# Kernel tuning notes

Hardware: AMD Instinct MI355X
Metric: run time of the kernel (lower is better)

Reference implementation:

```python
import jax, jax.numpy as jnp
import numpy as np

B, L, F, H, DIM = 32, 1024, 1024, 1024, 1024


def setup_inputs() -> dict:
    key = jax.random.key(0)
    ks = jax.random.split(key, 8)
    features = jax.random.normal(ks[0], (B, L, F), dtype=jnp.float32)
    hidden = jax.random.normal(ks[1], (B, H), dtype=jnp.float32)
    # Dense layer params (glorot-ish scale)
    W1 = jax.random.normal(ks[2], (F, DIM), dtype=jnp.float32) / np.sqrt(F)
    b1 = jnp.zeros((DIM,), dtype=jnp.float32)
    W2 = jax.random.normal(ks[3], (H, DIM), dtype=jnp.float32) / np.sqrt(H)
    b2 = jnp.zeros((DIM,), dtype=jnp.float32)
    Wp = jax.random.normal(ks[4], (DIM, 1), dtype=jnp.float32) / np.sqrt(DIM)
    bp = jnp.zeros((1,), dtype=jnp.float32)
    return {"features": features, "hidden": hidden, "W1": W1, "b1": b1,
            "W2": W2, "b2": b2, "Wp": Wp, "bp": bp}


def reference(features, hidden, W1, b1, W2, b2, Wp, bp):
    # features: [B, L, F], hidden: [B, H]
    h1 = jnp.einsum('blf,fd->bld', features, W1) + b1          # [B, L, D]
    h2 = (hidden @ W2 + b2)[:, None, :]                         # [B, 1, D]
    att = jnp.tanh(h1 + h2)                                     # [B, L, D]
    score = jnp.einsum('bld,do->blo', att, Wp) + bp             # [B, L, 1]
    attention_weights = jax.nn.softmax(score, axis=1)           # [B, L, 1]
    context_vector = jnp.sum(attention_weights * features, axis=1)  # [B, F]
    return context_vector
```

## Files before the change

### kernel.cpp

```cpp
#include <hip/hip_runtime.h>
#include <hip/hip_bf16.h>


typedef __attribute__((ext_vector_type(8))) __bf16 bf16x8;
typedef __attribute__((ext_vector_type(4))) float f32x4;

#define BM 128
#define BN 128
#define BK 32

static __device__ __forceinline__ ushort f2bf(float x) {
  unsigned u = __float_as_uint(x);
  return (ushort)((u + 0x7fffu + ((u >> 16) & 1u)) >> 16);
}

typedef __attribute__((address_space(1))) void gbl_t;
typedef __attribute__((address_space(3))) void lds_t;
static __device__ __forceinline__ void gl_lds16(const void* g, void* l) {
  __builtin_amdgcn_global_load_lds((gbl_t*)g, (lds_t*)l, 16, 0, 0);
}

static __device__ __forceinline__ bf16x8 cvt8(float4 lo, float4 hi) {
  __hip_bfloat162 c0 = __float22bfloat162_rn({lo.x, lo.y});
  __hip_bfloat162 c1 = __float22bfloat162_rn({lo.z, lo.w});
  __hip_bfloat162 c2 = __float22bfloat162_rn({hi.x, hi.y});
  __hip_bfloat162 c3 = __float22bfloat162_rn({hi.z, hi.w});
  union { int4 i; bf16x8 v; } u;
  u.i.x = *(int*)&c0; u.i.y = *(int*)&c1; u.i.z = *(int*)&c2; u.i.w = *(int*)&c3;
  return u.v;
}

__global__ __launch_bounds__(256) void transpose_w1_kernel(
    const float* __restrict__ W1, ushort* __restrict__ W1T) {
  __shared__ float t[64][65];
  const int tr = blockIdx.y, tc = blockIdx.x, tid = threadIdx.x;
  const int r = tid >> 4;
  const int c4 = (tid & 15) * 4;
#pragma unroll
  for (int p = 0; p < 4; ++p) {
    const int rr = p * 16 + r;
    float4 v = *(const float4*)(W1 + (size_t)(tr * 64 + rr) * 1024 + tc * 64 + c4);
    t[rr][c4] = v.x; t[rr][c4 + 1] = v.y; t[rr][c4 + 2] = v.z; t[rr][c4 + 3] = v.w;
  }
  __syncthreads();
  const int cc = tid >> 3;
  const int r8 = (tid & 7) * 8;
#pragma unroll
  for (int p = 0; p < 2; ++p) {
    const int c = p * 32 + cc;
    ushort tmp[8];
#pragma unroll
    for (int j = 0; j < 8; ++j) tmp[j] = f2bf(t[r8 + j][c]);
    *(int4*)(W1T + (size_t)(tc * 64 + c) * 1024 + tr * 64 + r8) = *(int4*)tmp;
  }
}

__global__ void zero_kernel(float* __restrict__ p) {
  p[(size_t)blockIdx.x * 256 + threadIdx.x] = 0.f;
}

__global__ __launch_bounds__(256) void h2_kernel(
    const float* __restrict__ hidden, const float* __restrict__ W2,
    const float* __restrict__ b2, float* __restrict__ h2p) {
  const int d = blockIdx.x * 256 + threadIdx.x;
  const int b = blockIdx.y;
  const int z = blockIdx.z;
  const int k0 = z * 128;
  __shared__ float h[128];
  if (threadIdx.x < 128) h[threadIdx.x] = hidden[b * 1024 + k0 + threadIdx.x];
  __syncthreads();
  float acc = (z == 0) ? b2[d] : 0.f;
#pragma unroll 8
  for (int k = 0; k < 128; ++k)
    acc += h[k] * W2[(size_t)(k0 + k) * 1024 + d];
  h2p[z * 32768 + b * 1024 + d] = acc;
}

__global__ __launch_bounds__(256) void gemm_score_kernel(
    const float* __restrict__ feat,
    const ushort* __restrict__ w1t,
    const float* __restrict__ b1,
    const float* __restrict__ h2p,
    const float* __restrict__ wp,
    float* __restrict__ score_p) {
  __shared__ float ldsA[BM * BK];
  __shared__ ushort ldsB[BN * BK];
  __shared__ float sred[2][64];
  const int tid = threadIdx.x;
  const int row0 = blockIdx.x * BM;
  const int col0 = blockIdx.y * BN;
  const int b = row0 >> 10;

  const int wave = tid >> 6, lane = tid & 63;
  const int wm = wave & 1, wn = wave >> 1;
  const int lrow = lane & 15;
  const int quad = lane >> 4;

  int a_go[4], a_ls[4];
#pragma unroll
  for (int it = 0; it < 4; ++it) {
    const int slot = wave * 256 + it * 64 + lane;
    const int r = slot >> 3, kc = slot & 7;
    a_go[it] = (row0 + r) * 1024 + (kc ^ (r & 7)) * 4;
    a_ls[it] = (wave * 256 + it * 64) * 16;
  }
  int b_go[2], b_ls[2];
#pragma unroll
  for (int it = 0; it < 2; ++it) {
    const int slot = wave * 128 + it * 64 + lane;
    const int r = slot >> 2, kc = slot & 3;
    b_go[it] = (col0 + r) * 1024 + (kc ^ ((r >> 1) & 3)) * 8;
    b_ls[it] = (wave * 128 + it * 64) * 16;
  }

  f32x4 acc[4][4] = {};

  for (int k0 = 0; k0 < 1024; k0 += BK) {
#pragma unroll
    for (int it = 0; it < 4; ++it)
      gl_lds16(feat + a_go[it] + k0, (char*)ldsA + a_ls[it]);
#pragma unroll
    for (int it = 0; it < 2; ++it)
      gl_lds16(w1t + b_go[it] + k0, (char*)ldsB + b_ls[it]);
    __syncthreads();

    bf16x8 af[4], bfr[4];
#pragma unroll
    for (int i = 0; i < 4; ++i) {
      const int r = wm * 64 + i * 16 + lrow;
      const int s0 = (quad * 2) ^ (r & 7);
      const int s1 = (quad * 2 + 1) ^ (r & 7);
      float4 lo = *(const float4*)&ldsA[r * 32 + s0 * 4];
      float4 hi = *(const float4*)&ldsA[r * 32 + s1 * 4];
      af[i] = cvt8(lo, hi);
    }
#pragma unroll
    for (int j = 0; j < 4; ++j) {
      const int r = wn * 64 + j * 16 + lrow;
      const int s = quad ^ ((r >> 1) & 3);
      bfr[j] = *(const bf16x8*)&ldsB[r * 32 + s * 8];
    }
#pragma unroll
    for (int i = 0; i < 4; ++i)
#pragma unroll
      for (int j = 0; j < 4; ++j)
        acc[i][j] = __builtin_amdgcn_mfma_f32_16x16x32_bf16(
            af[i], bfr[j], acc[i][j], 0, 0, 0);
    __syncthreads();
  }

  float hbv[4], wpv[4];
#pragma unroll
  for (int j = 0; j < 4; ++j) {
    const int d = col0 + wn * 64 + j * 16 + lrow;
    float hv = b1[d];
#pragma unroll
    for (int p = 0; p < 8; ++p) hv += h2p[p * 32768 + b * 1024 + d];
    hbv[j] = hv;
    wpv[j] = wp[d];
  }
  float rsum[4][4];
#pragma unroll
  for (int i = 0; i < 4; ++i) {
#pragma unroll
    for (int r = 0; r < 4; ++r) {
      float s = 0.f;
#pragma unroll
      for (int j = 0; j < 4; ++j)
        s += tanhf(acc[i][j][r] + hbv[j]) * wpv[j];
      s += __shfl_xor(s, 8);
      s += __shfl_xor(s, 4);
      s += __shfl_xor(s, 2);
      s += __shfl_xor(s, 1);
      rsum[i][r] = s;
    }
  }
  if (wn == 1 && lrow == 0) {
#pragma unroll
    for (int i = 0; i < 4; ++i)
#pragma unroll
      for (int r = 0; r < 4; ++r)
        sred[wm][i * 16 + quad * 4 + r] = rsum[i][r];
  }
  __syncthreads();
  if (wn == 0 && lrow == 0) {
#pragma unroll
    for (int i = 0; i < 4; ++i)
#pragma unroll
      for (int r = 0; r < 4; ++r) {
        const int ro = wm * 64 + i * 16 + quad * 4 + r;
        score_p[(size_t)blockIdx.y * 32768 + row0 + ro] =
            rsum[i][r] + sred[wm][ro & 63];
      }
  }
}

__global__ __launch_bounds__(256) void softmax_kernel(
    const float* __restrict__ score_p, float* __restrict__ w) {
  const int b = blockIdx.x, tid = threadIdx.x;
  const int lane = tid & 63, wv = tid >> 6;
  __shared__ float sm[4], ss[4];
  float v[4];
  float mx = -1e30f;
#pragma unroll
  for (int i = 0; i < 4; ++i) {
    const int idx = b * 1024 + i * 256 + tid;
    float s = 0.f;
#pragma unroll
    for (int p = 0; p < 8; ++p) s += score_p[p * 32768 + idx];
    v[i] = s;
    mx = fmaxf(mx, s);
  }
#pragma unroll
  for (int off = 32; off; off >>= 1) mx = fmaxf(mx, __shfl_xor(mx, off));
  if (lane == 0) sm[wv] = mx;
  __syncthreads();
  mx = fmaxf(fmaxf(sm[0], sm[1]), fmaxf(sm[2], sm[3]));
  float sum = 0.f;
#pragma unroll
  for (int i = 0; i < 4; ++i) {
    v[i] = __expf(v[i] - mx);
    sum += v[i];
  }
#pragma unroll
  for (int off = 32; off; off >>= 1) sum += __shfl_xor(sum, off);
  if (lane == 0) ss[wv] = sum;
  __syncthreads();
  const float inv = 1.f / (ss[0] + ss[1] + ss[2] + ss[3]);
#pragma unroll
  for (int i = 0; i < 4; ++i) w[b * 1024 + i * 256 + tid] = v[i] * inv;
}

__global__ __launch_bounds__(256) void context_kernel(
    const float* __restrict__ w, const float* __restrict__ feat,
    float* __restrict__ out) {
  const int b = blockIdx.y;
  const int l0 = blockIdx.x * 32;
  const int f0 = threadIdx.x * 4;
  __shared__ float wl[32];
  if (threadIdx.x < 32) wl[threadIdx.x] = w[b * 1024 + l0 + threadIdx.x];
  __syncthreads();
  const float* fb = feat + (size_t)b * 1048576 + (size_t)l0 * 1024 + f0;
  float a0 = 0.f, a1 = 0.f, a2 = 0.f, a3 = 0.f;
#pragma unroll 8
  for (int l = 0; l < 32; ++l) {
    float4 v = *(const float4*)(fb + (size_t)l * 1024);
    const float wv = wl[l];
    a0 += wv * v.x;
    a1 += wv * v.y;
    a2 += wv * v.z;
    a3 += wv * v.w;
  }
  float* dst = out + b * 1024 + f0;
  atomicAdd(dst + 0, a0);
  atomicAdd(dst + 1, a1);
  atomicAdd(dst + 2, a2);
  atomicAdd(dst + 3, a3);
}

extern "C" void kernel_launch(void* const* d_in, const int* in_sizes, int n_in,
                              void* d_out, int out_size, void* d_ws, size_t ws_size,
                              hipStream_t stream) {
  const float* feat   = (const float*)d_in[0];
  const float* hidden = (const float*)d_in[1];
  const float* W1     = (const float*)d_in[2];
  const float* b1     = (const float*)d_in[3];
  const float* W2     = (const float*)d_in[4];
  const float* b2     = (const float*)d_in[5];
  const float* Wp     = (const float*)d_in[6];
  float* out = (float*)d_out;

  char* ws = (char*)d_ws;
  ushort* w1t    = (ushort*)ws;
  float* score_p = (float*)(ws + 2097152);
  float* h2p     = (float*)(ws + 3145728);
  float* wts     = (float*)(ws + 4194304);

  transpose_w1_kernel<<<dim3(16, 16), 256, 0, stream>>>(W1, w1t);
  h2_kernel<<<dim3(4, 32, 8), 256, 0, stream>>>(hidden, W2, b2, h2p);
  gemm_score_kernel<<<dim3(256, 8), 256, 0, stream>>>(feat, w1t, b1, h2p, Wp,
                                                      score_p);
  softmax_kernel<<<32, 256, 0, stream>>>(score_p, wts);
  zero_kernel<<<128, 256, 0, stream>>>(out);
  context_kernel<<<dim3(32, 32), 256, 0, stream>>>(wts, feat, out);
}
```

Measured before the change: 392.2 us.

## Pre-convert features to bf16 in chunks before GEMM, with register-convert fallback

Adds a pass that converts the fp32 features to bf16 in a workspace buffer, processed in two halves, so the score GEMM can stream bf16 A tiles straight into LDS with half the bytes and no per-tile conversion. When the workspace is too small, a fallback GEMM instead loads fp32 through registers, converts, and writes padded LDS rows. The extra conversion pass adds a full read of features plus a bf16 write, which costs memory traffic. The context kernel still re-reads the fp32 features.

```diff
diff --git a/kernel.cpp b/kernel.cpp
--- a/kernel.cpp
+++ b/kernel.cpp
@@ -8,6 +8,7 @@
 #define BM 128
 #define BN 128
 #define BK 32
+#define LDK 40
 
 static __device__ __forceinline__ ushort f2bf(float x) {
   unsigned u = __float_as_uint(x);
@@ -28,6 +29,17 @@
   union { int4 i; bf16x8 v; } u;
   u.i.x = *(int*)&c0; u.i.y = *(int*)&c1; u.i.z = *(int*)&c2; u.i.w = *(int*)&c3;
   return u.v;
+}
+
+__global__ __launch_bounds__(256) void cvt_feat_kernel(
+    const float* __restrict__ feat, ushort* __restrict__ featb) {
+  const size_t i8 = ((size_t)blockIdx.x * 256 + threadIdx.x) * 8;
+  float4 a = *(const float4*)(feat + i8);
+  float4 b = *(const float4*)(feat + i8 + 4);
+  ushort t[8];
+  t[0] = f2bf(a.x); t[1] = f2bf(a.y); t[2] = f2bf(a.z); t[3] = f2bf(a.w);
+  t[4] = f2bf(b.x); t[5] = f2bf(b.y); t[6] = f2bf(b.z); t[7] = f2bf(b.w);
+  *(int4*)(featb + i8) = *(int4*)t;
 }
 
 __global__ __launch_bounds__(256) void transpose_w1_kernel(
@@ -76,69 +88,96 @@
   h2p[z * 32768 + b * 1024 + d] = acc;
 }
 
-__global__ __launch_bounds__(256) void gemm_score_kernel(
-    const float* __restrict__ feat,
+#define GEMM_EPILOGUE(ROWG)                                                    \
+  float hbv[4], wpv[4];                                                        \
+  _Pragma("unroll") for (int j = 0; j < 4; ++j) {                              \
+    const int d = col0 + wn * 64 + j * 16 + lrow;                              \
+    float hv = b1[d];                                                          \
+    _Pragma("unroll") for (int p = 0; p < 8; ++p)                              \
+        hv += h2p[p * 32768 + b * 1024 + d];                                   \
+    hbv[j] = hv;                                                               \
+    wpv[j] = wp[d];                                                            \
+  }                                                                            \
+  float rsum[4][4];                                                            \
+  _Pragma("unroll") for (int i = 0; i < 4; ++i) {                              \
+    _Pragma("unroll") for (int r = 0; r < 4; ++r) {                            \
+      float s = 0.f;                                                           \
+      _Pragma("unroll") for (int j = 0; j < 4; ++j)                            \
+          s += tanhf(acc[i][j][r] + hbv[j]) * wpv[j];                          \
+      s += __shfl_xor(s, 8);                                                   \
+      s += __shfl_xor(s, 4);                                                   \
+      s += __shfl_xor(s, 2);                                                   \
+      s += __shfl_xor(s, 1);                                                   \
+      rsum[i][r] = s;                                                          \
+    }                                                                          \
+  }                                                                            \
+  if (wn == 1 && lrow == 0) {                                                  \
+    _Pragma("unroll") for (int i = 0; i < 4; ++i)                              \
+        _Pragma("unroll") for (int r = 0; r < 4; ++r)                          \
+            sred[wm][i * 16 + quad * 4 + r] = rsum[i][r];                      \
+  }                                                                            \
+  __syncthreads();                                                             \
+  if (wn == 0 && lrow == 0) {                                                  \
+    _Pragma("unroll") for (int i = 0; i < 4; ++i)                              \
+        _Pragma("unroll") for (int r = 0; r < 4; ++r) {                        \
+          const int ro = wm * 64 + i * 16 + quad * 4 + r;                      \
+          score_p[(size_t)blockIdx.y * 32768 + (ROWG) + ro] =                  \
+              rsum[i][r] + sred[wm][ro & 63];                                  \
+        }                                                                      \
+  }
+
+__global__ __launch_bounds__(256) void gemm_score_bf16_kernel(
+    const ushort* __restrict__ featb,
     const ushort* __restrict__ w1t,
-    const float* __restrict__ b1,
-    const float* __restrict__ h2p,
-    const float* __restrict__ wp,
-    float* __restrict__ score_p) {
-  __shared__ float ldsA[BM * BK];
+    const float* __restrict__ b1, const float* __restrict__ h2p,
+    const float* __restrict__ wp, float* __restrict__ score_p,
+    int row_base) {
+  __shared__ ushort ldsA[BM * BK];
   __shared__ ushort ldsB[BN * BK];
   __shared__ float sred[2][64];
   const int tid = threadIdx.x;
   const int row0 = blockIdx.x * BM;
   const int col0 = blockIdx.y * BN;
-  const int b = row0 >> 10;
+  const int b = (row_base + row0) >> 10;
 
   const int wave = tid >> 6, lane = tid & 63;
   const int wm = wave & 1, wn = wave >> 1;
-  const int lrow = lane & 15;
-  const int quad = lane >> 4;
-
-  int a_go[4], a_ls[4];
-#pragma unroll
-  for (int it = 0; it < 4; ++it) {
-    const int slot = wave * 256 + it * 64 + lane;
-    const int r = slot >> 3, kc = slot & 7;
-    a_go[it] = (row0 + r) * 1024 + (kc ^ (r & 7)) * 4;
-    a_ls[it] = (wave * 256 + it * 64) * 16;
-  }
-  int b_go[2], b_ls[2];
+  const int lrow = lane & 15, quad = lane >> 4;
+
+  int a_go[2], b_go[2], ls[2];
 #pragma unroll
   for (int it = 0; it < 2; ++it) {
     const int slot = wave * 128 + it * 64 + lane;
     const int r = slot >> 2, kc = slot & 3;
-    b_go[it] = (col0 + r) * 1024 + (kc ^ ((r >> 1) & 3)) * 8;
-    b_ls[it] = (wave * 128 + it * 64) * 16;
+    const int swz = (r & 3) ^ ((r >> 2) & 3);
+    a_go[it] = (row0 + r) * 1024 + (kc ^ swz) * 8;
+    b_go[it] = (col0 + r) * 1024 + (kc ^ swz) * 8;
+    ls[it] = (wave * 128 + it * 64) * 16;
   }
 
   f32x4 acc[4][4] = {};
 
   for (int k0 = 0; k0 < 1024; k0 += BK) {
 #pragma unroll
-    for (int it = 0; it < 4; ++it)
-      gl_lds16(feat + a_go[it] + k0, (char*)ldsA + a_ls[it]);
-#pragma unroll
     for (int it = 0; it < 2; ++it)
-      gl_lds16(w1t + b_go[it] + k0, (char*)ldsB + b_ls[it]);
+      gl_lds16(featb + a_go[it] + k0, (char*)ldsA + ls[it]);
+#pragma unroll
+    for (int it = 0; it < 2; ++it)
+      gl_lds16(w1t + b_go[it] + k0, (char*)ldsB + ls[it]);
     __syncthreads();
 
     bf16x8 af[4], bfr[4];
 #pragma unroll
     for (int i = 0; i < 4; ++i) {
       const int r = wm * 64 + i * 16 + lrow;
-      const int s0 = (quad * 2) ^ (r & 7);
-      const int s1 = (quad * 2 + 1) ^ (r & 7);
-      float4 lo = *(const float4*)&ldsA[r * 32 + s0 * 4];
-      float4 hi = *(const float4*)&ldsA[r * 32 + s1 * 4];
-      af[i] = cvt8(lo, hi);
+      const int swz = (r & 3) ^ ((r >> 2) & 3);
+      af[i] = *(const bf16x8*)&ldsA[r * 32 + (quad ^ swz) * 8];
     }
 #pragma unroll
     for (int j = 0; j < 4; ++j) {
       const int r = wn * 64 + j * 16 + lrow;
-      const int s = quad ^ ((r >> 1) & 3);
-      bfr[j] = *(const bf16x8*)&ldsB[r * 32 + s * 8];
+      const int swz = (r & 3) ^ ((r >> 2) & 3);
+      bfr[j] = *(const bf16x8*)&ldsB[r * 32 + (quad ^ swz) * 8];
     }
 #pragma unroll
     for (int i = 0; i < 4; ++i)
@@ -149,50 +188,70 @@
     __syncthreads();
   }
 
-  float hbv[4], wpv[4];
-#pragma unroll
-  for (int j = 0; j < 4; ++j) {
-    const int d = col0 + wn * 64 + j * 16 + lrow;
-    float hv = b1[d];
-#pragma unroll
-    for (int p = 0; p < 8; ++p) hv += h2p[p * 32768 + b * 1024 + d];
-    hbv[j] = hv;
-    wpv[j] = wp[d];
-  }
-  float rsum[4][4];
-#pragma unroll
-  for (int i = 0; i < 4; ++i) {
-#pragma unroll
-    for (int r = 0; r < 4; ++r) {
-      float s = 0.f;
+  GEMM_EPILOGUE(row_base + row0)
+}
+
+__global__ __launch_bounds__(256) void gemm_score_cvt_kernel(
+    const float* __restrict__ feat,
+    const ushort* __restrict__ w1t, const float* __restrict__ b1,
+    const float* __restrict__ h2p, const float* __restrict__ wp,
+    float* __restrict__ score_p) {
+  __shared__ ushort ldsA[BM * LDK];
+  __shared__ ushort ldsB[BN * LDK];
+  __shared__ float sred[2][64];
+  const int tid = threadIdx.x;
+  const int row0 = blockIdx.x * BM;
+  const int col0 = blockIdx.y * BN;
+  const int b = row0 >> 10;
+
+  const int wave = tid >> 6, lane = tid & 63;
+  const int wm = wave & 1, wn = wave >> 1;
+  const int lrow = lane & 15, quad = lane >> 4;
+
+  const int arow = tid >> 1;
+  const int akof = (tid & 1) * 16;
+  const int brow = tid >> 2;
+  const int bkof = (tid & 3) * 8;
+
+  f32x4 acc[4][4] = {};
+
+  for (int k0 = 0; k0 < 1024; k0 += BK) {
+    {
+      const float* ap = feat + (size_t)(row0 + arow) * 1024 + k0 + akof;
+      float4 v0 = *(const float4*)(ap + 0);
+      float4 v1 = *(const float4*)(ap + 4);
+      float4 v2 = *(const float4*)(ap + 8);
+      float4 v3 = *(const float4*)(ap + 12);
+      union { bf16x8 v; int4 i; } w0, w1;
+      w0.v = cvt8(v0, v1);
+      w1.v = cvt8(v2, v3);
+      *(int4*)&ldsA[arow * LDK + akof] = w0.i;
+      *(int4*)&ldsA[arow * LDK + akof + 8] = w1.i;
+    }
+#pragma unroll
+    for (int p = 0; p < 2; ++p) {
+      const int m = p * 64 + brow;
+      *(int4*)&ldsB[m * LDK + bkof] =
+          *(const int4*)(w1t + (size_t)(col0 + m) * 1024 + k0 + bkof);
+    }
+    __syncthreads();
+    bf16x8 af[4], bfr[4];
+#pragma unroll
+    for (int i = 0; i < 4; ++i)
+      af[i] = *(const bf16x8*)&ldsA[(wm * 64 + i * 16 + lrow) * LDK + quad * 8];
+#pragma unroll
+    for (int j = 0; j < 4; ++j)
+      bfr[j] = *(const bf16x8*)&ldsB[(wn * 64 + j * 16 + lrow) * LDK + quad * 8];
+#pragma unroll
+    for (int i = 0; i < 4; ++i)
 #pragma unroll
       for (int j = 0; j < 4; ++j)
-        s += tanhf(acc[i][j][r] + hbv[j]) * wpv[j];
-      s += __shfl_xor(s, 8);
-      s += __shfl_xor(s, 4);
-      s += __shfl_xor(s, 2);
-      s += __shfl_xor(s, 1);
-      rsum[i][r] = s;
-    }
-  }
-  if (wn == 1 && lrow == 0) {
-#pragma unroll
-    for (int i = 0; i < 4; ++i)
-#pragma unroll
-      for (int r = 0; r < 4; ++r)
-        sred[wm][i * 16 + quad * 4 + r] = rsum[i][r];
-  }
-  __syncthreads();
-  if (wn == 0 && lrow == 0) {
-#pragma unroll
-    for (int i = 0; i < 4; ++i)
-#pragma unroll
-      for (int r = 0; r < 4; ++r) {
-        const int ro = wm * 64 + i * 16 + quad * 4 + r;
-        score_p[(size_t)blockIdx.y * 32768 + row0 + ro] =
-            rsum[i][r] + sred[wm][ro & 63];
-      }
-  }
+        acc[i][j] = __builtin_amdgcn_mfma_f32_16x16x32_bf16(
+            af[i], bfr[j], acc[i][j], 0, 0, 0);
+    __syncthreads();
+  }
+
+  GEMM_EPILOGUE(row0)
 }
 
 __global__ __launch_bounds__(256) void softmax_kernel(
@@ -275,11 +334,24 @@
   float* score_p = (float*)(ws + 2097152);
   float* h2p     = (float*)(ws + 3145728);
   float* wts     = (float*)(ws + 4194304);
+  ushort* featb  = (ushort*)(ws + 4325376);
+  const bool big_ws = ws_size >= (size_t)(4325376 + 33554432);
 
   transpose_w1_kernel<<<dim3(16, 16), 256, 0, stream>>>(W1, w1t);
   h2_kernel<<<dim3(4, 32, 8), 256, 0, stream>>>(hidden, W2, b2, h2p);
-  gemm_score_kernel<<<dim3(256, 8), 256, 0, stream>>>(feat, w1t, b1, h2p, Wp,
-                                                      score_p);
+
+  if (big_ws) {
+    for (int h = 0; h < 2; ++h) {
+      cvt_feat_kernel<<<8192, 256, 0, stream>>>(feat + (size_t)h * 16777216,
+                                                featb);
+      gemm_score_bf16_kernel<<<dim3(128, 8), 256, 0, stream>>>(
+          featb, w1t, b1, h2p, Wp, score_p, h * 16384);
+    }
+  } else {
+    gemm_score_cvt_kernel<<<dim3(256, 8), 256, 0, stream>>>(feat, w1t, b1, h2p,
+                                                            Wp, score_p);
+  }
+
   softmax_kernel<<<32, 256, 0, stream>>>(score_p, wts);
   zero_kernel<<<128, 256, 0, stream>>>(out);
   context_kernel<<<dim3(32, 32), 256, 0, stream>>>(wts, feat, out);
```

Measured after the change: 373.4 us. -4.8%, faster.
